# Performance work log

Measured on AMD Instinct MI355X. Metric: run time of the kernel, lower is better.

Reference implementation:

```python
import jax, jax.numpy as jnp
import numpy as np

N_FEATURES = 128
N_ACTIONS = 16
HIDDEN = 256
BATCH = 4096
IN_DIM = N_FEATURES + N_ACTIONS  # 144


def setup_inputs() -> dict:
    key = jax.random.key(0)
    k1, k2, k3, k4 = jax.random.split(key, 4)
    f_t = jax.random.normal(k1, (BATCH, N_FEATURES), dtype=jnp.float32)
    a_t = jax.random.normal(k2, (BATCH, N_ACTIONS), dtype=jnp.float32)
    # Stacked per-feature MLP params (one small MLP per output feature).
    W1 = jax.random.normal(k3, (N_FEATURES, IN_DIM, HIDDEN), dtype=jnp.float32) / np.sqrt(IN_DIM)
    b1 = jnp.zeros((N_FEATURES, HIDDEN), dtype=jnp.float32)
    W2 = jax.random.normal(k4, (N_FEATURES, HIDDEN), dtype=jnp.float32) / np.sqrt(HIDDEN)
    b2 = jnp.zeros((N_FEATURES,), dtype=jnp.float32)
    return {"f_t": f_t, "a_t": a_t, "W1": W1, "b1": b1, "W2": W2, "b2": b2}


def reference(f_t, a_t, W1, b1, W2, b2):
    # fa_t: [B, F+A] shared input to all per-feature models
    fa_t = jnp.concatenate((f_t, a_t), axis=1)
    # Grouped GEMM replacing parallel_apply over n_features tiny MLPs:
    # h: [M, B, H]
    h = jax.nn.relu(jnp.einsum('bi,mih->mbh', fa_t, W1) + b1[:, None, :])
    # out: [B, M]  (each model emits a single scalar per example)
    out = jnp.einsum('mbh,mh->bm', h, W2) + b2[None, :]
    # skip_connection=True, additional=False, all=False -> add f_t
    return out + f_t
```

## Files before the change

### kernel.cpp

```cpp
#include <hip/hip_runtime.h>
#include <hip/hip_bf16.h>

#define BATCH   4096
#define NF      128
#define NA      16
#define IN_DIM  144
#define KP      144
#define NKC     18
#define HID     256

typedef __attribute__((ext_vector_type(8))) short bf16x8;
typedef __attribute__((ext_vector_type(4))) float f32x4;
typedef __attribute__((ext_vector_type(16))) float f32x16;

__global__ void convert_all(const float* __restrict__ W1,
                            const float* __restrict__ f_t,
                            const float* __restrict__ a_t,
                            __hip_bfloat16* __restrict__ w1t,
                            __hip_bfloat16* __restrict__ fab2) {
    const int bid = blockIdx.x;
    const int t = threadIdx.x;
    if (bid < 1152) {
        __shared__ float tile[16][HID];
        int m = bid / 9;
        int kc = bid - m * 9;
        int k0 = kc * 16;
#pragma unroll
        for (int i = 0; i < 16; ++i)
            tile[i][t] = W1[((size_t)m * IN_DIM + (k0 + i)) * HID + t];
        __syncthreads();
        union { ushort us[16]; uint4 q[2]; } pk;
#pragma unroll
        for (int i = 0; i < 16; ++i) {
            __hip_bfloat16 h = __float2bfloat16(tile[i][t]);
            pk.us[i] = *(ushort*)&h;
        }
        uint4* dst = (uint4*)(w1t + ((size_t)m * HID + t) * KP + k0);
        dst[0] = pk.q[0];
        dst[1] = pk.q[1];
    } else {
        int b2i = bid - 1152;
        int cc = b2i / 16;
        int rb = b2i - cc * 16;
        int row = rb * 256 + t;
        union { ushort us[8]; uint4 q; } pk;
        const float* src = (cc < 16) ? (f_t + (size_t)row * NF + cc * 8)
                                     : (a_t + (size_t)row * NA + (cc - 16) * 8);
#pragma unroll
        for (int j = 0; j < 8; ++j) {
            __hip_bfloat16 h = __float2bfloat16(src[j]);
            pk.us[j] = *(ushort*)&h;
        }
        *(uint4*)(fab2 + ((size_t)cc * BATCH + row) * 8) = pk.q;
    }
}

__global__ __launch_bounds__(256, 2) void fused_mlp(
        const __hip_bfloat16* __restrict__ fab2,
        const __hip_bfloat16* __restrict__ w1t,
        const float* __restrict__ b1,
        const float* __restrict__ W2,
        const float* __restrict__ b2,
        const float* __restrict__ f_t,
        float* __restrict__ out) {
    __shared__ __align__(16) float partial[16][4][64];

    const int bid = blockIdx.x;
    const int m     = bid & 127;
    const int slice = bid >> 7;
    const int row_base = slice * 1024;
    const int t = threadIdx.x;
    const int w = t >> 6;
    const int lane = t & 63;
    const int l31 = lane & 31;
    const int h = lane >> 5;

    bf16x8 bfrag[2][9];
#pragma unroll
    for (int hi2 = 0; hi2 < 2; ++hi2) {
        const int col = w * 64 + hi2 * 32 + l31;
        const __hip_bfloat16* wp = w1t + ((size_t)m * HID + col) * KP + h * 8;
#pragma unroll
        for (int ks = 0; ks < 9; ++ks)
            bfrag[hi2][ks] = *(const bf16x8*)(wp + ks * 16);
    }
    f32x16 w2v[2], b1v[2];
#pragma unroll
    for (int hi2 = 0; hi2 < 2; ++hi2) {
        const float* wp2 = W2 + (size_t)m * HID + w * 64 + hi2 * 32 + 4 * h;
        const float* bp1 = b1 + (size_t)m * HID + w * 64 + hi2 * 32 + 4 * h;
#pragma unroll
        for (int q = 0; q < 4; ++q) {
            f32x4 v = *(const f32x4*)(wp2 + 8 * q);
            f32x4 bv = *(const f32x4*)(bp1 + 8 * q);
#pragma unroll
            for (int i = 0; i < 4; ++i) {
                w2v[hi2][q * 4 + i] = v[i];
                b1v[hi2][q * 4 + i] = bv[i];
            }
        }
    }
    const float b2v = b2[m];

    for (int tile = 0; tile < 16; ++tile) {
        const int r0 = row_base + tile * 64;
        const __hip_bfloat16* fb0 = fab2 + ((size_t)h * BATCH + r0 + l31) * 8;
        const __hip_bfloat16* fb1 = fb0 + 32 * 8;

        f32x16 acc[2][2];

        {
            bf16x8 a0 = *(const bf16x8*)fb0;
            bf16x8 a1 = *(const bf16x8*)fb1;
#pragma unroll
            for (int hi2 = 0; hi2 < 2; ++hi2) {
                acc[hi2][0] = __builtin_amdgcn_mfma_f32_32x32x16_bf16(
                    bfrag[hi2][0], a0, b1v[hi2], 0, 0, 0);
                acc[hi2][1] = __builtin_amdgcn_mfma_f32_32x32x16_bf16(
                    bfrag[hi2][0], a1, b1v[hi2], 0, 0, 0);
            }
        }
#pragma unroll
        for (int ks = 1; ks < 9; ++ks) {
            bf16x8 a0 = *(const bf16x8*)(fb0 + (size_t)ks * 2 * BATCH * 8);
            bf16x8 a1 = *(const bf16x8*)(fb1 + (size_t)ks * 2 * BATCH * 8);
#pragma unroll
            for (int hi2 = 0; hi2 < 2; ++hi2) {
                acc[hi2][0] = __builtin_amdgcn_mfma_f32_32x32x16_bf16(
                    bfrag[hi2][ks], a0, acc[hi2][0], 0, 0, 0);
                acc[hi2][1] = __builtin_amdgcn_mfma_f32_32x32x16_bf16(
                    bfrag[hi2][ks], a1, acc[hi2][1], 0, 0, 0);
            }
        }

        float sarr[2];
#pragma unroll
        for (int bj2 = 0; bj2 < 2; ++bj2) {
            float sr0 = 0.f, sr1 = 0.f, sr2 = 0.f, sr3 = 0.f;
#pragma unroll
            for (int hi2 = 0; hi2 < 2; ++hi2)
#pragma unroll
                for (int q = 0; q < 4; ++q) {
                    float h0 = acc[hi2][bj2][q*4+0]; h0 = h0 > 0.f ? h0 : 0.f;
                    float h1 = acc[hi2][bj2][q*4+1]; h1 = h1 > 0.f ? h1 : 0.f;
                    float h2 = acc[hi2][bj2][q*4+2]; h2 = h2 > 0.f ? h2 : 0.f;
                    float h3 = acc[hi2][bj2][q*4+3]; h3 = h3 > 0.f ? h3 : 0.f;
                    sr0 = fmaf(h0, w2v[hi2][q*4+0], sr0);
                    sr1 = fmaf(h1, w2v[hi2][q*4+1], sr1);
                    sr2 = fmaf(h2, w2v[hi2][q*4+2], sr2);
                    sr3 = fmaf(h3, w2v[hi2][q*4+3], sr3);
                }
            float s = (sr0 + sr1) + (sr2 + sr3);
            s += __shfl_xor(s, 32, 64);
            sarr[bj2] = s;
        }
        if (h == 0) {
            partial[tile][w][l31]      = sarr[0];
            partial[tile][w][32 + l31] = sarr[1];
        }
    }

    __syncthreads();
#pragma unroll
    for (int i = 0; i < 4; ++i) {
        int idx = i * 256 + t;
        int tl = idx >> 6;
        int r  = idx & 63;
        int row = row_base + tl * 64 + r;
        float v = (partial[tl][0][r] + partial[tl][1][r])
                + (partial[tl][2][r] + partial[tl][3][r])
                + b2v + f_t[(size_t)row * NF + m];
        out[(size_t)row * NF + m] = v;
    }
}

extern "C" void kernel_launch(void* const* d_in, const int* in_sizes, int n_in,
                              void* d_out, int out_size, void* d_ws, size_t ws_size,
                              hipStream_t stream) {
    const float* f_t = (const float*)d_in[0];
    const float* a_t = (const float*)d_in[1];
    const float* W1  = (const float*)d_in[2];
    const float* b1  = (const float*)d_in[3];
    const float* W2  = (const float*)d_in[4];
    const float* b2  = (const float*)d_in[5];
    float* out = (float*)d_out;

    __hip_bfloat16* w1t  = (__hip_bfloat16*)d_ws;
    __hip_bfloat16* fab2 = (__hip_bfloat16*)((char*)d_ws + (size_t)NF * HID * KP * 2);

    hipLaunchKernelGGL(convert_all, dim3(1440), dim3(256), 0, stream,
                       W1, f_t, a_t, w1t, fab2);
    hipLaunchKernelGGL(fused_mlp, dim3(512), dim3(256), 0, stream,
                       fab2, w1t, b1, W2, b2, f_t, out);
}
```

Baseline: 59.72 us.

## Double-buffer activation fragment loads across 32-row tiles in fused MLP

Restructures the main loop of the fused MLP kernel to work on 32-row tiles with two register buffers. The next tile's activation fragments are prefetched while the MFMA chain and reduction for the current tile run. The goal is to hide global load latency behind the MFMA work. In exchange it uses more registers for the prefetch buffers and keeps only one independent accumulator chain per hi2, which lowers MFMA-level parallelism and could hurt occupancy under launch_bounds(256,2).

```diff
diff --git a/kernel.cpp b/kernel.cpp
--- a/kernel.cpp
+++ b/kernel.cpp
@@ -6,7 +6,6 @@
 #define NA      16
 #define IN_DIM  144
 #define KP      144
-#define NKC     18
 #define HID     256
 
 typedef __attribute__((ext_vector_type(8))) short bf16x8;
@@ -63,7 +62,7 @@
         const float* __restrict__ b2,
         const float* __restrict__ f_t,
         float* __restrict__ out) {
-    __shared__ __align__(16) float partial[16][4][64];
+    __shared__ __align__(16) float partial[32][4][32];
 
     const int bid = blockIdx.x;
     const int m     = bid & 127;
@@ -102,71 +101,68 @@
     }
     const float b2v = b2[m];
 
-    for (int tile = 0; tile < 16; ++tile) {
-        const int r0 = row_base + tile * 64;
-        const __hip_bfloat16* fb0 = fab2 + ((size_t)h * BATCH + r0 + l31) * 8;
-        const __hip_bfloat16* fb1 = fb0 + 32 * 8;
+    const __hip_bfloat16* fbase = fab2 + ((size_t)h * BATCH + l31) * 8;
 
-        f32x16 acc[2][2];
+#define LOADT(BUF, RR)                                                        \
+    {                                                                         \
+        const __hip_bfloat16* fb = fbase + (size_t)(RR) * 8;                  \
+        _Pragma("unroll")                                                     \
+        for (int ks = 0; ks < 9; ++ks)                                        \
+            BUF[ks] = *(const bf16x8*)(fb + (size_t)ks * 2 * BATCH * 8);      \
+    }
 
-        {
-            bf16x8 a0 = *(const bf16x8*)fb0;
-            bf16x8 a1 = *(const bf16x8*)fb1;
-#pragma unroll
-            for (int hi2 = 0; hi2 < 2; ++hi2) {
-                acc[hi2][0] = __builtin_amdgcn_mfma_f32_32x32x16_bf16(
-                    bfrag[hi2][0], a0, b1v[hi2], 0, 0, 0);
-                acc[hi2][1] = __builtin_amdgcn_mfma_f32_32x32x16_bf16(
-                    bfrag[hi2][0], a1, b1v[hi2], 0, 0, 0);
-            }
-        }
-#pragma unroll
-        for (int ks = 1; ks < 9; ++ks) {
-            bf16x8 a0 = *(const bf16x8*)(fb0 + (size_t)ks * 2 * BATCH * 8);
-            bf16x8 a1 = *(const bf16x8*)(fb1 + (size_t)ks * 2 * BATCH * 8);
-#pragma unroll
-            for (int hi2 = 0; hi2 < 2; ++hi2) {
-                acc[hi2][0] = __builtin_amdgcn_mfma_f32_32x32x16_bf16(
-                    bfrag[hi2][ks], a0, acc[hi2][0], 0, 0, 0);
-                acc[hi2][1] = __builtin_amdgcn_mfma_f32_32x32x16_bf16(
-                    bfrag[hi2][ks], a1, acc[hi2][1], 0, 0, 0);
-            }
-        }
+#define COMPT(BUF, TL)                                                        \
+    {                                                                         \
+        f32x16 acc[2];                                                        \
+        _Pragma("unroll")                                                     \
+        for (int hi2 = 0; hi2 < 2; ++hi2)                                     \
+            acc[hi2] = __builtin_amdgcn_mfma_f32_32x32x16_bf16(               \
+                bfrag[hi2][0], BUF[0], b1v[hi2], 0, 0, 0);                    \
+        _Pragma("unroll")                                                     \
+        for (int ks = 1; ks < 9; ++ks)                                        \
+            _Pragma("unroll")                                                 \
+            for (int hi2 = 0; hi2 < 2; ++hi2)                                 \
+                acc[hi2] = __builtin_amdgcn_mfma_f32_32x32x16_bf16(           \
+                    bfrag[hi2][ks], BUF[ks], acc[hi2], 0, 0, 0);              \
+        float sr0 = 0.f, sr1 = 0.f, sr2 = 0.f, sr3 = 0.f;                     \
+        _Pragma("unroll")                                                     \
+        for (int hi2 = 0; hi2 < 2; ++hi2)                                     \
+            _Pragma("unroll")                                                 \
+            for (int q = 0; q < 4; ++q) {                                     \
+                float h0 = acc[hi2][q*4+0]; h0 = h0 > 0.f ? h0 : 0.f;         \
+                float h1 = acc[hi2][q*4+1]; h1 = h1 > 0.f ? h1 : 0.f;         \
+                float h2 = acc[hi2][q*4+2]; h2 = h2 > 0.f ? h2 : 0.f;         \
+                float h3 = acc[hi2][q*4+3]; h3 = h3 > 0.f ? h3 : 0.f;         \
+                sr0 = fmaf(h0, w2v[hi2][q*4+0], sr0);                         \
+                sr1 = fmaf(h1, w2v[hi2][q*4+1], sr1);                         \
+                sr2 = fmaf(h2, w2v[hi2][q*4+2], sr2);                         \
+                sr3 = fmaf(h3, w2v[hi2][q*4+3], sr3);                         \
+            }                                                                 \
+        float s = (sr0 + sr1) + (sr2 + sr3);                                  \
+        s += __shfl_xor(s, 32, 64);                                           \
+        if (h == 0) partial[TL][w][l31] = s;                                  \
+    }
 
-        float sarr[2];
-#pragma unroll
-        for (int bj2 = 0; bj2 < 2; ++bj2) {
-            float sr0 = 0.f, sr1 = 0.f, sr2 = 0.f, sr3 = 0.f;
-#pragma unroll
-            for (int hi2 = 0; hi2 < 2; ++hi2)
-#pragma unroll
-                for (int q = 0; q < 4; ++q) {
-                    float h0 = acc[hi2][bj2][q*4+0]; h0 = h0 > 0.f ? h0 : 0.f;
-                    float h1 = acc[hi2][bj2][q*4+1]; h1 = h1 > 0.f ? h1 : 0.f;
-                    float h2 = acc[hi2][bj2][q*4+2]; h2 = h2 > 0.f ? h2 : 0.f;
-                    float h3 = acc[hi2][bj2][q*4+3]; h3 = h3 > 0.f ? h3 : 0.f;
-                    sr0 = fmaf(h0, w2v[hi2][q*4+0], sr0);
-                    sr1 = fmaf(h1, w2v[hi2][q*4+1], sr1);
-                    sr2 = fmaf(h2, w2v[hi2][q*4+2], sr2);
-                    sr3 = fmaf(h3, w2v[hi2][q*4+3], sr3);
-                }
-            float s = (sr0 + sr1) + (sr2 + sr3);
-            s += __shfl_xor(s, 32, 64);
-            sarr[bj2] = s;
-        }
-        if (h == 0) {
-            partial[tile][w][l31]      = sarr[0];
-            partial[tile][w][32 + l31] = sarr[1];
-        }
+    bf16x8 bufA[9], bufB[9];
+    LOADT(bufA, row_base);
+#pragma unroll 4
+    for (int tp = 0; tp < 16; ++tp) {
+        const int t0 = 2 * tp;
+        LOADT(bufB, row_base + (t0 + 1) * 32);
+        COMPT(bufA, t0);
+        if (t0 + 2 < 32) LOADT(bufA, row_base + (t0 + 2) * 32);
+        COMPT(bufB, t0 + 1);
     }
+#undef LOADT
+#undef COMPT
 
     __syncthreads();
 #pragma unroll
     for (int i = 0; i < 4; ++i) {
         int idx = i * 256 + t;
-        int tl = idx >> 6;
-        int r  = idx & 63;
-        int row = row_base + tl * 64 + r;
+        int tl = idx >> 5;
+        int r  = idx & 31;
+        int row = row_base + tl * 32 + r;
         float v = (partial[tl][0][r] + partial[tl][1][r])
                 + (partial[tl][2][r] + partial[tl][3][r])
                 + b2v + f_t[(size_t)row * NF + m];
```

Measured after the change: 57.19 us. 4.2% less time.
